# Kernel optimization log

Measured on AMD Instinct MI355X. Metric: run time of the kernel, lower is better.

## Reference

```python
import jax, jax.numpy as jnp
import numpy as np

# ---- constants (from init_kwargs / Config) ----
C = 10            # number of classes
P = 128           # fixed prototype capacity per class (masked)
GAMMA = 0.1
B_CONST = 10.0    # b
TAO = 1.0
BETA = 1.0
LAMBDA = 0.1
THRESHOLD = 40.0
EPS = 1e-6        # nn.PairwiseDistance eps (added to the difference)


def setup_inputs() -> dict:
    key = jax.random.key(0)
    k1, k2 = jax.random.split(key)
    features = jax.random.normal(k1, (8192, 512), dtype=jnp.float32)
    labels = jax.random.randint(k2, (8192,), 0, C, dtype=jnp.int32)
    return {"features": features, "labels": labels}


def _assign_prototypes(features, labels):
    """Sequential prototype assignment (faithful to assign_prototype).
    Fixed-capacity store: protos [C,P,D], counts [C,P], nproto [C]."""
    D = features.shape[1]
    protos = jnp.zeros((C, P, D), features.dtype)
    counts = jnp.zeros((C, P), jnp.int32)
    nproto = jnp.zeros((C,), jnp.int32)

    def step(carry, xs):
        protos, counts, nproto = carry
        f, l = xs
        row = protos[l]                       # [P, D]
        cnt = counts[l]                       # [P]
        n = nproto[l]
        valid = jnp.arange(P) < n
        d2 = jnp.sum((f[None, :] - row + EPS) ** 2, axis=-1)
        d2m = jnp.where(valid, d2, jnp.inf)
        idx = jnp.argmin(d2m)
        dmin = jnp.sqrt(d2m[idx])
        do_update = (n > 0) & (dmin < THRESHOLD)
        # running-mean update of closest prototype
        c = cnt[idx].astype(f.dtype)
        new_val = (row[idx] * c + f) / (c + 1.0)
        app_idx = jnp.minimum(n, P - 1)       # append slot (clamped; never hit with these settings)
        tgt_idx = jnp.where(do_update, idx, app_idx)
        tgt_val = jnp.where(do_update, new_val, f)
        tgt_cnt = jnp.where(do_update, cnt[idx] + 1, 1)
        row = row.at[tgt_idx].set(tgt_val)
        cnt = cnt.at[tgt_idx].set(tgt_cnt)
        n = jnp.where(do_update, n, jnp.minimum(n + 1, P))
        protos = protos.at[l].set(row)
        counts = counts.at[l].set(cnt)
        nproto = nproto.at[l].set(n)
        return (protos, counts, nproto), None

    (protos, counts, nproto), _ = jax.lax.scan(step, (protos, counts, nproto), (features, labels))
    return protos, nproto


def _forward(features, labels):
    # assign_prototype uses tensor(features).detach() -> stop_gradient
    protos, nproto = _assign_prototypes(jax.lax.stop_gradient(features), labels)
    B, D = features.shape
    flat = protos.reshape(C * P, D)
    valid = (jnp.arange(P)[None, :] < nproto[:, None]).reshape(C * P)

    # squared PairwiseDistance with eps added to the difference:
    # sum((f - p + eps)^2) = |f|^2 + |p|^2 - 2 f.p + 2*eps*(sum f - sum p) + D*eps^2
    f2 = jnp.sum(features ** 2, axis=-1)          # [B]
    p2 = jnp.sum(flat ** 2, axis=-1)              # [C*P]
    sf = jnp.sum(features, axis=-1)
    sp = jnp.sum(flat, axis=-1)
    d2 = (f2[:, None] + p2[None, :] - 2.0 * (features @ flat.T)
          + 2.0 * EPS * (sf[:, None] - sp[None, :]) + D * EPS * EPS)
    d2 = jnp.maximum(d2, 0.0)                     # [B, C*P]

    # dce loss: probability = 1e-6 + sum_label exp(-g d^2) / sum_all exp(-g d^2)
    expv = jnp.where(valid[None, :], jnp.exp(-GAMMA * d2), 0.0)
    per_class = expv.reshape(B, C, P).sum(-1)     # [B, C]
    one = per_class.sum(-1)                       # [B]
    num = jnp.take_along_axis(per_class, labels[:, None].astype(jnp.int32), axis=1)[:, 0]
    prob = 1e-6 + jnp.where(one > 0.0, num / one, one)
    dce_loss = jnp.sum(-jnp.log(prob))

    # pairwise loss: per sample, per existing class, min distance
    d2c = jnp.where(valid[None, :], d2, jnp.inf).reshape(B, C, P).min(-1)
    dmin = jnp.sqrt(d2c)                          # [B, C]
    sign = jnp.where(labels[:, None] == jnp.arange(C)[None, :], 1.0, -1.0)
    z = B_CONST - (TAO - dmin) * sign
    g = jnp.where(z > 10.0, z, jax.nn.softplus(BETA * z) / BETA)
    exists = nproto > 0                           # only classes present in all_prototypes
    pw_loss = jnp.sum(jnp.where(exists[None, :], g, 0.0))

    return dce_loss + LAMBDA * pw_loss


def reference(features, labels):
    return _forward(features, labels)
```

## Files before the change

### kernel.cpp

```cpp
#include <hip/hip_runtime.h>
#include <math.h>

#define NC 10
#define NP 128
#define ND 512
#define GAMMA  0.1f
#define BCONST 10.0f
#define TAO    1.0f
#define LAMBDA 0.1f
#define THR2   1600.0f
#define FEPS   1e-6f
#define NLDS   12
#define CH     16
#define MAXCH  512
#define IMAX   0x7FFFFFFF

__device__ __forceinline__ float allred64(float v) {
#pragma unroll
  for (int m = 1; m < 64; m <<= 1) v += __shfl_xor(v, m, 64);
  return v;
}

__global__ __launch_bounds__(256)
void ord_kernel(const int* __restrict__ labels, int B,
                int* __restrict__ order, int* __restrict__ cls_base,
                int* __restrict__ cls_cnt, int* __restrict__ fail_pos,
                int* __restrict__ nproto_g, float* __restrict__ out)
{
  __shared__ int lab[8192];
  __shared__ int wtot[4][NC];
  const int t = threadIdx.x, lane = t & 63, w = t >> 6;

  if (t < NC) { fail_pos[t] = IMAX; nproto_g[t] = 0; }
  if (t == 0) out[0] = 0.f;

  const int4* lp = (const int4*)labels;
  for (int i = t; i < (B >> 2); i += 256) {
    int4 v = lp[i];
    lab[i*4+0] = v.x; lab[i*4+1] = v.y; lab[i*4+2] = v.z; lab[i*4+3] = v.w;
  }
  for (int i = (B & ~3) + t; i < B; i += 256) lab[i] = labels[i];
  __syncthreads();

  const int segsz = (B + 255) >> 8;
  const int s0 = t * segsz, s1 = min(s0 + segsz, B);

  int loc[NC];
#pragma unroll
  for (int c = 0; c < NC; ++c) loc[c] = 0;
  for (int i = s0; i < s1; ++i) {
    int l = lab[i];
#pragma unroll
    for (int c = 0; c < NC; ++c) loc[c] += (l == c) ? 1 : 0;
  }

  int pre[NC];
#pragma unroll
  for (int c = 0; c < NC; ++c) pre[c] = loc[c];
#pragma unroll
  for (int m = 1; m < 64; m <<= 1) {
#pragma unroll
    for (int c = 0; c < NC; ++c) {
      int u = __shfl_up(pre[c], m, 64);
      if (lane >= m) pre[c] += u;
    }
  }
  if (lane == 63) {
#pragma unroll
    for (int c = 0; c < NC; ++c) wtot[w][c] = pre[c];
  }
  __syncthreads();

  int pos[NC];
  {
    int cb = 0;
#pragma unroll
    for (int c = 0; c < NC; ++c) {
      int tot = wtot[0][c] + wtot[1][c] + wtot[2][c] + wtot[3][c];
      int before = 0;
#pragma unroll
      for (int ww = 0; ww < 4; ++ww) before += (ww < w) ? wtot[ww][c] : 0;
      pos[c] = cb + before + (pre[c] - loc[c]);
      if (t == 0) { cls_base[c] = cb; cls_cnt[c] = tot; }
      cb += tot;
    }
  }

  for (int i = s0; i < s1; ++i) {
    int l = lab[i];
#pragma unroll
    for (int c = 0; c < NC; ++c)
      if (l == c) order[pos[c]++] = i;
  }
}

__global__ __launch_bounds__(64)
void chunksum_kernel(const float* __restrict__ feats, const int* __restrict__ order,
                     const int* __restrict__ cls_base, const int* __restrict__ cls_cnt,
                     float* __restrict__ chunksum)
{
  const int c = blockIdx.x / MAXCH, g = blockIdx.x % MAXCH;
  const int cnt = cls_cnt[c];
  const int nch = (cnt + CH - 1) / CH;
  if (g >= nch) return;
  const int base = cls_base[c], lane = threadIdx.x;
  const int k0 = g * CH, k1 = min(k0 + CH, cnt);
  int myidx = (lane < CH && k0 + lane < cnt) ? order[base + k0 + lane] : 0;

  float S[8] = {0, 0, 0, 0, 0, 0, 0, 0};
  int k = k0;
  for (; k + 4 <= k1; k += 4) {
    float4 A[4], Bv[4];
#pragma unroll
    for (int j = 0; j < 4; ++j) {
      int idx = __shfl(myidx, k + j - k0, 64);
      const float4* fp = (const float4*)(feats + (size_t)idx * ND + lane * 8);
      A[j] = fp[0]; Bv[j] = fp[1];
    }
#pragma unroll
    for (int j = 0; j < 4; ++j) {
      S[0]+=A[j].x; S[1]+=A[j].y; S[2]+=A[j].z; S[3]+=A[j].w;
      S[4]+=Bv[j].x; S[5]+=Bv[j].y; S[6]+=Bv[j].z; S[7]+=Bv[j].w;
    }
  }
  for (; k < k1; ++k) {
    int idx = __shfl(myidx, k - k0, 64);
    const float4* fp = (const float4*)(feats + (size_t)idx * ND + lane * 8);
    float4 a = fp[0], b = fp[1];
    S[0]+=a.x; S[1]+=a.y; S[2]+=a.z; S[3]+=a.w;
    S[4]+=b.x; S[5]+=b.y; S[6]+=b.z; S[7]+=b.w;
  }
  float4* cp = (float4*)(chunksum + ((size_t)c * MAXCH + g) * ND + lane * 8);
  cp[0] = make_float4(S[0], S[1], S[2], S[3]);
  cp[1] = make_float4(S[4], S[5], S[6], S[7]);
}

__global__ __launch_bounds__(64)
void verify_kernel(const float* __restrict__ feats, const int* __restrict__ order,
                   const int* __restrict__ cls_base, const int* __restrict__ cls_cnt,
                   const float* __restrict__ chunksum, int* __restrict__ fail_pos,
                   float* __restrict__ gproto, float* __restrict__ p2s,
                   float* __restrict__ sps, int* __restrict__ nproto_g)
{
  const int c = blockIdx.x / MAXCH, g = blockIdx.x % MAXCH;
  const int cnt = cls_cnt[c];
  const int nch = (cnt + CH - 1) / CH;
  if (g >= nch) return;
  const int base = cls_base[c], lane = threadIdx.x;
  const int k0 = g * CH, k1 = min(k0 + CH, cnt);
  int myidx = (lane < CH && k0 + lane < cnt) ? order[base + k0 + lane] : 0;

  float P[8] = {0, 0, 0, 0, 0, 0, 0, 0};
  {
    const float* cbase = chunksum + (size_t)c * MAXCH * ND + lane * 8;
    int j = 0;
    for (; j + 4 <= g; j += 4) {
      float4 A[4], Bv[4];
#pragma unroll
      for (int q = 0; q < 4; ++q) {
        const float4* pp = (const float4*)(cbase + (size_t)(j + q) * ND);
        A[q] = pp[0]; Bv[q] = pp[1];
      }
#pragma unroll
      for (int q = 0; q < 4; ++q) {
        P[0]+=A[q].x; P[1]+=A[q].y; P[2]+=A[q].z; P[3]+=A[q].w;
        P[4]+=Bv[q].x; P[5]+=Bv[q].y; P[6]+=Bv[q].z; P[7]+=Bv[q].w;
      }
    }
    for (; j < g; ++j) {
      const float4* pp = (const float4*)(cbase + (size_t)j * ND);
      float4 a = pp[0], b = pp[1];
      P[0]+=a.x; P[1]+=a.y; P[2]+=a.z; P[3]+=a.w;
      P[4]+=b.x; P[5]+=b.y; P[6]+=b.z; P[7]+=b.w;
    }
  }

  int k = k0;
  for (; k + 4 <= k1; k += 4) {
    float4 A[4], Bv[4];
#pragma unroll
    for (int j = 0; j < 4; ++j) {
      int idx = __shfl(myidx, k + j - k0, 64);
      const float4* fp = (const float4*)(feats + (size_t)idx * ND + lane * 8);
      A[j] = fp[0]; Bv[j] = fp[1];
    }
    float part[4];
#pragma unroll
    for (int j = 0; j < 4; ++j) {
      int kk = k + j;
      float f[8] = {A[j].x, A[j].y, A[j].z, A[j].w, Bv[j].x, Bv[j].y, Bv[j].z, Bv[j].w};
      if (kk > 0) {
        float inv = 1.f / (float)kk;
        float p = 0.f;
#pragma unroll
        for (int e = 0; e < 8; ++e) { float d = f[e] - P[e] * inv + FEPS; p += d * d; }
        part[j] = p;
      } else part[j] = 0.f;
#pragma unroll
      for (int e = 0; e < 8; ++e) P[e] += f[e];
    }
#pragma unroll
    for (int m = 1; m < 64; m <<= 1) {
#pragma unroll
      for (int j = 0; j < 4; ++j) part[j] += __shfl_xor(part[j], m, 64);
    }
    if (lane == 0) {
#pragma unroll
      for (int j = 0; j < 4; ++j) {
        int kk = k + j;
        if (kk > 0 && !(part[j] < THR2)) atomicMin(&fail_pos[c], kk);
      }
    }
  }
  for (; k < k1; ++k) {
    int idx = __shfl(myidx, k - k0, 64);
    const float4* fp = (const float4*)(feats + (size_t)idx * ND + lane * 8);
    float4 fa = fp[0], fb = fp[1];
    float f[8] = {fa.x, fa.y, fa.z, fa.w, fb.x, fb.y, fb.z, fb.w};
    if (k > 0) {
      float inv = 1.f / (float)k;
      float p = 0.f;
#pragma unroll
      for (int e = 0; e < 8; ++e) { float d = f[e] - P[e] * inv + FEPS; p += d * d; }
      float d2 = allred64(p);
      if (!(d2 < THR2) && lane == 0) atomicMin(&fail_pos[c], k);
    }
#pragma unroll
    for (int e = 0; e < 8; ++e) P[e] += f[e];
  }

  if (g == nch - 1) {
    float inv = 1.f / (float)cnt;
    float p[8];
#pragma unroll
    for (int e = 0; e < 8; ++e) p[e] = P[e] * inv;
    float4* gp = (float4*)(gproto + (size_t)c * NP * ND + lane * 8);
    gp[0] = make_float4(p[0], p[1], p[2], p[3]);
    gp[1] = make_float4(p[4], p[5], p[6], p[7]);
    float P2p = 0.f, SPp = 0.f;
#pragma unroll
    for (int e = 0; e < 8; ++e) { P2p += p[e]*p[e]; SPp += p[e]; }
    float P2 = allred64(P2p), SP = allred64(SPp);
    if (lane == 0) { p2s[c*NP] = P2; sps[c*NP] = SP; nproto_g[c] = 1; }
  }
}

__global__ __launch_bounds__(64)
void fallback_kernel(const float* __restrict__ feats, const int* __restrict__ order,
                     const int* __restrict__ cls_base, const int* __restrict__ cls_cnt,
                     const int* __restrict__ fail_pos,
                     float* __restrict__ gproto, float* __restrict__ p2s,
                     float* __restrict__ sps, int* __restrict__ nproto_g)
{
  const int c = blockIdx.x;
  if (fail_pos[c] == IMAX) return;

  __shared__ float ls_proto[NLDS][ND];
  __shared__ int   ls_cnt[NP];
  const int lane = threadIdx.x;
  const int base = cls_base[c], cnt = cls_cnt[c];

  float p0[8];
  int cnt0 = 0, n = 0;
  float fA[8], fB[8], fC[8];

  auto LOADF = [&](float (&buf)[8], int m) {
    int idx = order[base + m];
    const float4* fp = (const float4*)(feats + (size_t)idx * ND + lane * 8);
    float4 a = fp[0], b = fp[1];
    buf[0]=a.x; buf[1]=a.y; buf[2]=a.z; buf[3]=a.w;
    buf[4]=b.x; buf[5]=b.y; buf[6]=b.z; buf[7]=b.w;
  };

  auto STEP = [&](float (&f)[8]) {
    float best = 3.4e38f;
    int bidx = 0;
    if (n > 0) {
      float part = 0.f;
#pragma unroll
      for (int e = 0; e < 8; ++e) { float d = f[e] - p0[e] + FEPS; part += d * d; }
      best = allred64(part);
      for (int j = 1; j < n; ++j) {
        float pj[8];
        if (j <= NLDS) {
          const float4* pp = (const float4*)(&ls_proto[j-1][lane*8]);
          float4 a = pp[0], b = pp[1];
          pj[0]=a.x; pj[1]=a.y; pj[2]=a.z; pj[3]=a.w;
          pj[4]=b.x; pj[5]=b.y; pj[6]=b.z; pj[7]=b.w;
        } else {
          const float4* pp = (const float4*)(gproto + ((size_t)c*NP + j)*ND + lane*8);
          float4 a = pp[0], b = pp[1];
          pj[0]=a.x; pj[1]=a.y; pj[2]=a.z; pj[3]=a.w;
          pj[4]=b.x; pj[5]=b.y; pj[6]=b.z; pj[7]=b.w;
        }
        float part2 = 0.f;
#pragma unroll
        for (int e = 0; e < 8; ++e) { float d = f[e] - pj[e] + FEPS; part2 += d * d; }
        float tot = allred64(part2);
        if (tot < best) { best = tot; bidx = j; }
      }
    }
    if (n > 0 && best < THR2) {
      if (bidx == 0) {
        float cc = (float)cnt0, inv = 1.f / (cc + 1.f);
#pragma unroll
        for (int e = 0; e < 8; ++e) p0[e] = (p0[e]*cc + f[e]) * inv;
        cnt0++;
      } else {
        int ci = ls_cnt[bidx];
        float cc = (float)ci, inv = 1.f / (cc + 1.f);
        if (bidx <= NLDS) {
          float* row = &ls_proto[bidx-1][lane*8];
#pragma unroll
          for (int e = 0; e < 8; ++e) row[e] = (row[e]*cc + f[e]) * inv;
        } else {
          float* row = gproto + ((size_t)c*NP + bidx)*ND + lane*8;
#pragma unroll
          for (int e = 0; e < 8; ++e) row[e] = (row[e]*cc + f[e]) * inv;
        }
        if (lane == 0) ls_cnt[bidx] = ci + 1;
      }
    } else {
      int app = min(n, NP - 1);
      if (app == 0) {
#pragma unroll
        for (int e = 0; e < 8; ++e) p0[e] = f[e];
        cnt0 = 1;
      } else if (app <= NLDS) {
        float* row = &ls_proto[app-1][lane*8];
#pragma unroll
        for (int e = 0; e < 8; ++e) row[e] = f[e];
        if (lane == 0) ls_cnt[app] = 1;
      } else {
        float* row = gproto + ((size_t)c*NP + app)*ND + lane*8;
#pragma unroll
        for (int e = 0; e < 8; ++e) row[e] = f[e];
        if (lane == 0) ls_cnt[app] = 1;
      }
      n = min(n + 1, NP);
    }
  };

  if (cnt > 0) LOADF(fA, 0);
  if (cnt > 1) LOADF(fB, 1);
  if (cnt > 2) LOADF(fC, 2);
  int m = 0;
  while (m < cnt) {
    STEP(fA); ++m; if (m + 2 < cnt) LOADF(fA, m + 2);
    if (m >= cnt) break;
    STEP(fB); ++m; if (m + 2 < cnt) LOADF(fB, m + 2);
    if (m >= cnt) break;
    STEP(fC); ++m; if (m + 2 < cnt) LOADF(fC, m + 2);
  }

  for (int j = 0; j < n; ++j) {
    float pj[8];
    if (j == 0) {
#pragma unroll
      for (int e = 0; e < 8; ++e) pj[e] = p0[e];
    } else if (j <= NLDS) {
      const float4* pp = (const float4*)(&ls_proto[j-1][lane*8]);
      float4 a = pp[0], b = pp[1];
      pj[0]=a.x; pj[1]=a.y; pj[2]=a.z; pj[3]=a.w;
      pj[4]=b.x; pj[5]=b.y; pj[6]=b.z; pj[7]=b.w;
    } else {
      const float4* pp = (const float4*)(gproto + ((size_t)c*NP + j)*ND + lane*8);
      float4 a = pp[0], b = pp[1];
      pj[0]=a.x; pj[1]=a.y; pj[2]=a.z; pj[3]=a.w;
      pj[4]=b.x; pj[5]=b.y; pj[6]=b.z; pj[7]=b.w;
    }
    float4* gp = (float4*)(gproto + ((size_t)c*NP + j)*ND + lane*8);
    gp[0] = make_float4(pj[0], pj[1], pj[2], pj[3]);
    gp[1] = make_float4(pj[4], pj[5], pj[6], pj[7]);
    float P2p = 0.f, SPp = 0.f;
#pragma unroll
    for (int e = 0; e < 8; ++e) { P2p += pj[e]*pj[e]; SPp += pj[e]; }
    float P2 = allred64(P2p), SP = allred64(SPp);
    if (lane == 0) { p2s[c*NP + j] = P2; sps[c*NP + j] = SP; }
  }
  if (lane == 0) nproto_g[c] = n;
}

__global__ __launch_bounds__(256)
void loss_kernel(const float* __restrict__ feats, const int* __restrict__ labels, int B,
                 const float* __restrict__ gproto, const float* __restrict__ p2s,
                 const float* __restrict__ sps, const int* __restrict__ nproto_g,
                 float* __restrict__ out)
{
  __shared__ float bsum[4];
  const int lane = threadIdx.x & 63;
  const int wid  = threadIdx.x >> 6;
  const int gw   = blockIdx.x * 4 + wid;
  const int nw   = gridDim.x * 4;

  int np[NC];
  bool fast = true;
#pragma unroll
  for (int cc = 0; cc < NC; ++cc) { np[cc] = nproto_g[cc]; fast &= (np[cc] == 1); }

  float acc = 0.f;

  if (fast) {
    float p2v[NC], spv[NC];
#pragma unroll
    for (int cc = 0; cc < NC; ++cc) { p2v[cc] = p2s[cc*NP]; spv[cc] = sps[cc*NP]; }

    for (int b = gw; b < B; b += nw) {
      const float4* fp = (const float4*)(feats + (size_t)b * ND + lane * 8);
      float4 a4 = fp[0], b4 = fp[1];
      float f[8] = {a4.x, a4.y, a4.z, a4.w, b4.x, b4.y, b4.z, b4.w};
      int lab = labels[b];

      float v[12];
#pragma unroll
      for (int cc = 0; cc < NC; ++cc) {
        const float4* pp = (const float4*)(gproto + (size_t)cc * NP * ND + lane * 8);
        float4 pa = pp[0], pb = pp[1];
        v[cc] = f[0]*pa.x + f[1]*pa.y + f[2]*pa.z + f[3]*pa.w
              + f[4]*pb.x + f[5]*pb.y + f[6]*pb.z + f[7]*pb.w;
      }
      float f2p = 0.f, sfp = 0.f;
#pragma unroll
      for (int e = 0; e < 8; ++e) { f2p += f[e]*f[e]; sfp += f[e]; }
      v[10] = f2p; v[11] = sfp;

#pragma unroll
      for (int m = 1; m < 64; m <<= 1) {
#pragma unroll
        for (int q = 0; q < 12; ++q) v[q] += __shfl_xor(v[q], m, 64);
      }
      float f2 = v[10], sf = v[11];

      float one = 0.f, num = 0.f, pw = 0.f;
#pragma unroll
      for (int cc = 0; cc < NC; ++cc) {
        float d2 = f2 + p2v[cc] - 2.f*v[cc]
                 + 2.f*FEPS*(sf - spv[cc]) + (float)ND*FEPS*FEPS;
        d2 = fmaxf(d2, 0.f);
        float e = expf(-GAMMA * d2);
        one += e;
        if (cc == lab) num = e;
        float dmin = sqrtf(d2);
        float sign = (cc == lab) ? 1.f : -1.f;
        float z = BCONST - (TAO - dmin) * sign;
        float gg = (z > 10.f) ? z : log1pf(expf(z));
        pw += gg;
      }
      float prob = 1e-6f + ((one > 0.f) ? num / one : one);
      acc += -logf(prob) + LAMBDA * pw;
    }
  } else {
    for (int b = gw; b < B; b += nw) {
      const float4* fp = (const float4*)(feats + (size_t)b * ND + lane * 8);
      float4 a4 = fp[0], b4 = fp[1];
      float f[8] = {a4.x, a4.y, a4.z, a4.w, b4.x, b4.y, b4.z, b4.w};
      float f2p = 0.f, sfp = 0.f;
#pragma unroll
      for (int e = 0; e < 8; ++e) { f2p += f[e]*f[e]; sfp += f[e]; }
      float f2 = allred64(f2p);
      float sf = allred64(sfp);
      int lab = labels[b];

      float one = 0.f, num = 0.f, pw = 0.f;
      for (int cc = 0; cc < NC; ++cc) {
        int nn = np[cc];
        if (nn <= 0) continue;
        float sume = 0.f, bestd2 = 3.4e38f;
        for (int j = 0; j < nn; ++j) {
          const float4* pp = (const float4*)(gproto + ((size_t)cc*NP + j)*ND + lane*8);
          float4 pa = pp[0], pb = pp[1];
          float dp = f[0]*pa.x + f[1]*pa.y + f[2]*pa.z + f[3]*pa.w
                   + f[4]*pb.x + f[5]*pb.y + f[6]*pb.z + f[7]*pb.w;
          float dot = allred64(dp);
          float d2 = f2 + p2s[cc*NP + j] - 2.f*dot
                   + 2.f*FEPS*(sf - sps[cc*NP + j]) + (float)ND*FEPS*FEPS;
          d2 = fmaxf(d2, 0.f);
          sume  += expf(-GAMMA * d2);
          bestd2 = fminf(bestd2, d2);
        }
        one += sume;
        if (cc == lab) num = sume;
        float dmin = sqrtf(bestd2);
        float sign = (cc == lab) ? 1.f : -1.f;
        float z = BCONST - (TAO - dmin) * sign;
        float g = (z > 10.f) ? z : log1pf(expf(z));
        pw += g;
      }
      float prob = 1e-6f + ((one > 0.f) ? num / one : one);
      acc += -logf(prob) + LAMBDA * pw;
    }
  }

  if (lane == 0) bsum[wid] = acc;
  __syncthreads();
  if (threadIdx.x == 0) atomicAdd(out, bsum[0] + bsum[1] + bsum[2] + bsum[3]);
}

extern "C" void kernel_launch(void* const* d_in, const int* in_sizes, int n_in,
                              void* d_out, int out_size, void* d_ws, size_t ws_size,
                              hipStream_t stream) {
  const float* feats  = (const float*)d_in[0];
  const int*   labels = (const int*)d_in[1];
  int B = in_sizes[0] / ND;

  float* gproto   = (float*)d_ws;
  float* p2s      = gproto + (size_t)NC * NP * ND;
  float* sps      = p2s + NC * NP;
  float* chunksum = sps + NC * NP;
  int*   nproto_g = (int*)(chunksum + (size_t)NC * MAXCH * ND);
  int*   order    = nproto_g + NC;
  int*   cls_base = order + B;
  int*   cls_cnt  = cls_base + NC;
  int*   fail_pos = cls_cnt + NC;

  hipLaunchKernelGGL(ord_kernel, dim3(1), dim3(256), 0, stream,
                     labels, B, order, cls_base, cls_cnt, fail_pos,
                     nproto_g, (float*)d_out);
  hipLaunchKernelGGL(chunksum_kernel, dim3(NC * MAXCH), dim3(64), 0, stream,
                     feats, order, cls_base, cls_cnt, chunksum);
  hipLaunchKernelGGL(verify_kernel, dim3(NC * MAXCH), dim3(64), 0, stream,
                     feats, order, cls_base, cls_cnt, chunksum, fail_pos,
                     gproto, p2s, sps, nproto_g);
  hipLaunchKernelGGL(fallback_kernel, dim3(NC), dim3(64), 0, stream,
                     feats, order, cls_base, cls_cnt, fail_pos,
                     gproto, p2s, sps, nproto_g);
  hipLaunchKernelGGL(loss_kernel, dim3(2048), dim3(256), 0, stream,
                     feats, labels, B, gproto, p2s, sps, nproto_g, (float*)d_out);
}
```

Before: 88.82 us.

## Fuse five-kernel pipeline into one cooperative persistent kernel with grid syncs

Replaces the five separate launches (ordering, chunk sums, verify, fallback, loss) with a single cooperative kernel of 256 blocks that separates the phases with grid.sync. Chunk work is compacted into a flat list indexed by per-class chunk bases, so no waves are spent on empty chunk slots. This removes launch gaps and idle blocks between phases. The cost is grid-wide barriers, only 1024 waves for the loss phase, and a serial ordering phase on block 0 while the other blocks wait. The old multi-kernel path stays as a fallback if the cooperative launch fails.

```diff
diff --git a/kernel.cpp b/kernel.cpp
--- a/kernel.cpp
+++ b/kernel.cpp
@@ -1,5 +1,8 @@
 #include <hip/hip_runtime.h>
+#include <hip/hip_cooperative_groups.h>
 #include <math.h>
+
+namespace cg = cooperative_groups;
 
 #define NC 10
 #define NP 128
@@ -14,11 +17,474 @@
 #define CH     16
 #define MAXCH  512
 #define IMAX   0x7FFFFFFF
-
-__device__ __forceinline__ float allred64(float v) {
+#define NBLK   256
+#define NWAVES (NBLK * 4)
+
+__device__ __forceinline__ float allredf(float v) {
 #pragma unroll
   for (int m = 1; m < 64; m <<= 1) v += __shfl_xor(v, m, 64);
   return v;
+}
+
+struct SOrd { int lab[8192]; int wtot[4][NC]; };
+struct SFb  { float ls_proto[NLDS][ND]; int ls_cnt[NP]; };
+union  SMem { SOrd ord; SFb fb; };
+
+__global__ __launch_bounds__(256, 2)
+void fused_kernel(const float* __restrict__ feats, const int* __restrict__ labels, int B,
+                  float* __restrict__ gproto, float* __restrict__ p2s, float* __restrict__ sps,
+                  float* __restrict__ chunksum,
+                  int* __restrict__ cls_base, int* __restrict__ cls_cnt,
+                  int* __restrict__ chunk_base, int* __restrict__ nchtot_g,
+                  int* __restrict__ fail_pos, int* __restrict__ nproto_g,
+                  int* __restrict__ order, float* __restrict__ out)
+{
+  cg::grid_group grid = cg::this_grid();
+  __shared__ SMem sm;
+  __shared__ float bsum[4];
+
+  const int t = threadIdx.x, lane = t & 63, wid = t >> 6;
+  const int gwid = blockIdx.x * 4 + wid;
+
+  if (blockIdx.x == 0) {
+    const int w = wid;
+    if (t < NC) { fail_pos[t] = IMAX; nproto_g[t] = 0; }
+    if (t == 0) out[0] = 0.f;
+
+    const int4* lp = (const int4*)labels;
+    for (int i = t; i < (B >> 2); i += 256) {
+      int4 v = lp[i];
+      sm.ord.lab[i*4+0] = v.x; sm.ord.lab[i*4+1] = v.y;
+      sm.ord.lab[i*4+2] = v.z; sm.ord.lab[i*4+3] = v.w;
+    }
+    for (int i = (B & ~3) + t; i < B; i += 256) sm.ord.lab[i] = labels[i];
+    __syncthreads();
+
+    const int segsz = (B + 255) >> 8;
+    const int s0 = t * segsz, s1 = min(s0 + segsz, B);
+
+    int loc[NC];
+#pragma unroll
+    for (int c = 0; c < NC; ++c) loc[c] = 0;
+    for (int i = s0; i < s1; ++i) {
+      int l = sm.ord.lab[i];
+#pragma unroll
+      for (int c = 0; c < NC; ++c) loc[c] += (l == c) ? 1 : 0;
+    }
+
+    int pre[NC];
+#pragma unroll
+    for (int c = 0; c < NC; ++c) pre[c] = loc[c];
+#pragma unroll
+    for (int m = 1; m < 64; m <<= 1) {
+#pragma unroll
+      for (int c = 0; c < NC; ++c) {
+        int u = __shfl_up(pre[c], m, 64);
+        if (lane >= m) pre[c] += u;
+      }
+    }
+    if (lane == 63) {
+#pragma unroll
+      for (int c = 0; c < NC; ++c) sm.ord.wtot[w][c] = pre[c];
+    }
+    __syncthreads();
+
+    int pos[NC];
+    {
+      int cb = 0, crun = 0;
+#pragma unroll
+      for (int c = 0; c < NC; ++c) {
+        int tot = sm.ord.wtot[0][c] + sm.ord.wtot[1][c] + sm.ord.wtot[2][c] + sm.ord.wtot[3][c];
+        int before = 0;
+#pragma unroll
+        for (int ww = 0; ww < 4; ++ww) before += (ww < w) ? sm.ord.wtot[ww][c] : 0;
+        pos[c] = cb + before + (pre[c] - loc[c]);
+        if (t == 0) { cls_base[c] = cb; cls_cnt[c] = tot; chunk_base[c] = crun; }
+        cb += tot;
+        crun += (tot + CH - 1) / CH;
+      }
+      if (t == 0) nchtot_g[0] = crun;
+    }
+
+    for (int i = s0; i < s1; ++i) {
+      int l = sm.ord.lab[i];
+#pragma unroll
+      for (int c = 0; c < NC; ++c)
+        if (l == c) order[pos[c]++] = i;
+    }
+  }
+  grid.sync();
+
+  int chbv[NC];
+#pragma unroll
+  for (int c = 0; c < NC; ++c) chbv[c] = chunk_base[c];
+  const int nchtot = nchtot_g[0];
+
+  for (int fid = gwid; fid < nchtot; fid += NWAVES) {
+    int c = 0;
+    while (c + 1 < NC && chbv[c + 1] <= fid) ++c;
+    const int g = fid - chbv[c];
+    const int cnt = cls_cnt[c], base = cls_base[c];
+    const int k0 = g * CH, k1 = min(k0 + CH, cnt);
+    int myidx = (lane < CH && k0 + lane < cnt) ? order[base + k0 + lane] : 0;
+
+    float S[8] = {0, 0, 0, 0, 0, 0, 0, 0};
+    int k = k0;
+    for (; k + 4 <= k1; k += 4) {
+      float4 A[4], Bv[4];
+#pragma unroll
+      for (int j = 0; j < 4; ++j) {
+        int idx = __shfl(myidx, k + j - k0, 64);
+        const float4* fp = (const float4*)(feats + (size_t)idx * ND + lane * 8);
+        A[j] = fp[0]; Bv[j] = fp[1];
+      }
+#pragma unroll
+      for (int j = 0; j < 4; ++j) {
+        S[0]+=A[j].x; S[1]+=A[j].y; S[2]+=A[j].z; S[3]+=A[j].w;
+        S[4]+=Bv[j].x; S[5]+=Bv[j].y; S[6]+=Bv[j].z; S[7]+=Bv[j].w;
+      }
+    }
+    for (; k < k1; ++k) {
+      int idx = __shfl(myidx, k - k0, 64);
+      const float4* fp = (const float4*)(feats + (size_t)idx * ND + lane * 8);
+      float4 a = fp[0], b = fp[1];
+      S[0]+=a.x; S[1]+=a.y; S[2]+=a.z; S[3]+=a.w;
+      S[4]+=b.x; S[5]+=b.y; S[6]+=b.z; S[7]+=b.w;
+    }
+    float4* cp = (float4*)(chunksum + (size_t)fid * ND + lane * 8);
+    cp[0] = make_float4(S[0], S[1], S[2], S[3]);
+    cp[1] = make_float4(S[4], S[5], S[6], S[7]);
+  }
+  grid.sync();
+
+  for (int fid = gwid; fid < nchtot; fid += NWAVES) {
+    int c = 0;
+    while (c + 1 < NC && chbv[c + 1] <= fid) ++c;
+    const int g = fid - chbv[c];
+    const int cnt = cls_cnt[c], base = cls_base[c];
+    const int nch = (cnt + CH - 1) / CH;
+    const int k0 = g * CH, k1 = min(k0 + CH, cnt);
+    int myidx = (lane < CH && k0 + lane < cnt) ? order[base + k0 + lane] : 0;
+
+    float P[8] = {0, 0, 0, 0, 0, 0, 0, 0};
+    {
+      const float* cbase = chunksum + (size_t)chbv[c] * ND + lane * 8;
+      int j = 0;
+      for (; j + 4 <= g; j += 4) {
+        float4 A[4], Bv[4];
+#pragma unroll
+        for (int q = 0; q < 4; ++q) {
+          const float4* pp = (const float4*)(cbase + (size_t)(j + q) * ND);
+          A[q] = pp[0]; Bv[q] = pp[1];
+        }
+#pragma unroll
+        for (int q = 0; q < 4; ++q) {
+          P[0]+=A[q].x; P[1]+=A[q].y; P[2]+=A[q].z; P[3]+=A[q].w;
+          P[4]+=Bv[q].x; P[5]+=Bv[q].y; P[6]+=Bv[q].z; P[7]+=Bv[q].w;
+        }
+      }
+      for (; j < g; ++j) {
+        const float4* pp = (const float4*)(cbase + (size_t)j * ND);
+        float4 a = pp[0], b = pp[1];
+        P[0]+=a.x; P[1]+=a.y; P[2]+=a.z; P[3]+=a.w;
+        P[4]+=b.x; P[5]+=b.y; P[6]+=b.z; P[7]+=b.w;
+      }
+    }
+
+    int k = k0;
+    for (; k + 4 <= k1; k += 4) {
+      float4 A[4], Bv[4];
+#pragma unroll
+      for (int j = 0; j < 4; ++j) {
+        int idx = __shfl(myidx, k + j - k0, 64);
+        const float4* fp = (const float4*)(feats + (size_t)idx * ND + lane * 8);
+        A[j] = fp[0]; Bv[j] = fp[1];
+      }
+      float part[4];
+#pragma unroll
+      for (int j = 0; j < 4; ++j) {
+        int kk = k + j;
+        float f[8] = {A[j].x, A[j].y, A[j].z, A[j].w, Bv[j].x, Bv[j].y, Bv[j].z, Bv[j].w};
+        if (kk > 0) {
+          float inv = 1.f / (float)kk;
+          float p = 0.f;
+#pragma unroll
+          for (int e = 0; e < 8; ++e) { float d = f[e] - P[e] * inv + FEPS; p += d * d; }
+          part[j] = p;
+        } else part[j] = 0.f;
+#pragma unroll
+        for (int e = 0; e < 8; ++e) P[e] += f[e];
+      }
+#pragma unroll
+      for (int m = 1; m < 64; m <<= 1) {
+#pragma unroll
+        for (int j = 0; j < 4; ++j) part[j] += __shfl_xor(part[j], m, 64);
+      }
+      if (lane == 0) {
+#pragma unroll
+        for (int j = 0; j < 4; ++j) {
+          int kk = k + j;
+          if (kk > 0 && !(part[j] < THR2)) atomicMin(&fail_pos[c], kk);
+        }
+      }
+    }
+    for (; k < k1; ++k) {
+      int idx = __shfl(myidx, k - k0, 64);
+      const float4* fp = (const float4*)(feats + (size_t)idx * ND + lane * 8);
+      float4 fa = fp[0], fb = fp[1];
+      float f[8] = {fa.x, fa.y, fa.z, fa.w, fb.x, fb.y, fb.z, fb.w};
+      if (k > 0) {
+        float inv = 1.f / (float)k;
+        float p = 0.f;
+#pragma unroll
+        for (int e = 0; e < 8; ++e) { float d = f[e] - P[e] * inv + FEPS; p += d * d; }
+        float d2 = allredf(p);
+        if (!(d2 < THR2) && lane == 0) atomicMin(&fail_pos[c], k);
+      }
+#pragma unroll
+      for (int e = 0; e < 8; ++e) P[e] += f[e];
+    }
+
+    if (g == nch - 1 && cnt > 0) {
+      float inv = 1.f / (float)cnt;
+      float p[8];
+#pragma unroll
+      for (int e = 0; e < 8; ++e) p[e] = P[e] * inv;
+      float4* gp = (float4*)(gproto + (size_t)c * NP * ND + lane * 8);
+      gp[0] = make_float4(p[0], p[1], p[2], p[3]);
+      gp[1] = make_float4(p[4], p[5], p[6], p[7]);
+      float P2p = 0.f, SPp = 0.f;
+#pragma unroll
+      for (int e = 0; e < 8; ++e) { P2p += p[e]*p[e]; SPp += p[e]; }
+      float P2 = allredf(P2p), SP = allredf(SPp);
+      if (lane == 0) { p2s[c*NP] = P2; sps[c*NP] = SP; nproto_g[c] = 1; }
+    }
+  }
+  grid.sync();
+
+  if (wid == 0 && blockIdx.x < NC && fail_pos[blockIdx.x] != IMAX) {
+    const int c = blockIdx.x;
+    const int base = cls_base[c], cnt = cls_cnt[c];
+    float p0[8];
+    int cnt0 = 0, n = 0;
+    float fA[8], fB[8], fC[8];
+
+    auto LOADF = [&](float (&buf)[8], int m) {
+      int idx = order[base + m];
+      const float4* fp = (const float4*)(feats + (size_t)idx * ND + lane * 8);
+      float4 a = fp[0], b = fp[1];
+      buf[0]=a.x; buf[1]=a.y; buf[2]=a.z; buf[3]=a.w;
+      buf[4]=b.x; buf[5]=b.y; buf[6]=b.z; buf[7]=b.w;
+    };
+    auto STEP = [&](float (&f)[8]) {
+      float best = 3.4e38f;
+      int bidx = 0;
+      if (n > 0) {
+        float part = 0.f;
+#pragma unroll
+        for (int e = 0; e < 8; ++e) { float d = f[e] - p0[e] + FEPS; part += d * d; }
+        best = allredf(part);
+        for (int j = 1; j < n; ++j) {
+          float pj[8];
+          if (j <= NLDS) {
+            const float4* pp = (const float4*)(&sm.fb.ls_proto[j-1][lane*8]);
+            float4 a = pp[0], b = pp[1];
+            pj[0]=a.x; pj[1]=a.y; pj[2]=a.z; pj[3]=a.w;
+            pj[4]=b.x; pj[5]=b.y; pj[6]=b.z; pj[7]=b.w;
+          } else {
+            const float4* pp = (const float4*)(gproto + ((size_t)c*NP + j)*ND + lane*8);
+            float4 a = pp[0], b = pp[1];
+            pj[0]=a.x; pj[1]=a.y; pj[2]=a.z; pj[3]=a.w;
+            pj[4]=b.x; pj[5]=b.y; pj[6]=b.z; pj[7]=b.w;
+          }
+          float part2 = 0.f;
+#pragma unroll
+          for (int e = 0; e < 8; ++e) { float d = f[e] - pj[e] + FEPS; part2 += d * d; }
+          float tot = allredf(part2);
+          if (tot < best) { best = tot; bidx = j; }
+        }
+      }
+      if (n > 0 && best < THR2) {
+        if (bidx == 0) {
+          float cc = (float)cnt0, inv = 1.f / (cc + 1.f);
+#pragma unroll
+          for (int e = 0; e < 8; ++e) p0[e] = (p0[e]*cc + f[e]) * inv;
+          cnt0++;
+        } else {
+          int ci = sm.fb.ls_cnt[bidx];
+          float cc = (float)ci, inv = 1.f / (cc + 1.f);
+          if (bidx <= NLDS) {
+            float* row = &sm.fb.ls_proto[bidx-1][lane*8];
+#pragma unroll
+            for (int e = 0; e < 8; ++e) row[e] = (row[e]*cc + f[e]) * inv;
+          } else {
+            float* row = gproto + ((size_t)c*NP + bidx)*ND + lane*8;
+#pragma unroll
+            for (int e = 0; e < 8; ++e) row[e] = (row[e]*cc + f[e]) * inv;
+          }
+          if (lane == 0) sm.fb.ls_cnt[bidx] = ci + 1;
+        }
+      } else {
+        int app = min(n, NP - 1);
+        if (app == 0) {
+#pragma unroll
+          for (int e = 0; e < 8; ++e) p0[e] = f[e];
+          cnt0 = 1;
+        } else if (app <= NLDS) {
+          float* row = &sm.fb.ls_proto[app-1][lane*8];
+#pragma unroll
+          for (int e = 0; e < 8; ++e) row[e] = f[e];
+          if (lane == 0) sm.fb.ls_cnt[app] = 1;
+        } else {
+          float* row = gproto + ((size_t)c*NP + app)*ND + lane*8;
+#pragma unroll
+          for (int e = 0; e < 8; ++e) row[e] = f[e];
+          if (lane == 0) sm.fb.ls_cnt[app] = 1;
+        }
+        n = min(n + 1, NP);
+      }
+    };
+
+    if (cnt > 0) LOADF(fA, 0);
+    if (cnt > 1) LOADF(fB, 1);
+    if (cnt > 2) LOADF(fC, 2);
+    int m = 0;
+    while (m < cnt) {
+      STEP(fA); ++m; if (m + 2 < cnt) LOADF(fA, m + 2);
+      if (m >= cnt) break;
+      STEP(fB); ++m; if (m + 2 < cnt) LOADF(fB, m + 2);
+      if (m >= cnt) break;
+      STEP(fC); ++m; if (m + 2 < cnt) LOADF(fC, m + 2);
+    }
+
+    for (int j = 0; j < n; ++j) {
+      float pj[8];
+      if (j == 0) {
+#pragma unroll
+        for (int e = 0; e < 8; ++e) pj[e] = p0[e];
+      } else if (j <= NLDS) {
+        const float4* pp = (const float4*)(&sm.fb.ls_proto[j-1][lane*8]);
+        float4 a = pp[0], b = pp[1];
+        pj[0]=a.x; pj[1]=a.y; pj[2]=a.z; pj[3]=a.w;
+        pj[4]=b.x; pj[5]=b.y; pj[6]=b.z; pj[7]=b.w;
+      } else {
+        const float4* pp = (const float4*)(gproto + ((size_t)c*NP + j)*ND + lane*8);
+        float4 a = pp[0], b = pp[1];
+        pj[0]=a.x; pj[1]=a.y; pj[2]=a.z; pj[3]=a.w;
+        pj[4]=b.x; pj[5]=b.y; pj[6]=b.z; pj[7]=b.w;
+      }
+      float4* gp = (float4*)(gproto + ((size_t)c*NP + j)*ND + lane*8);
+      gp[0] = make_float4(pj[0], pj[1], pj[2], pj[3]);
+      gp[1] = make_float4(pj[4], pj[5], pj[6], pj[7]);
+      float P2p = 0.f, SPp = 0.f;
+#pragma unroll
+      for (int e = 0; e < 8; ++e) { P2p += pj[e]*pj[e]; SPp += pj[e]; }
+      float P2 = allredf(P2p), SP = allredf(SPp);
+      if (lane == 0) { p2s[c*NP + j] = P2; sps[c*NP + j] = SP; }
+    }
+    if (lane == 0) nproto_g[c] = n;
+  }
+  grid.sync();
+
+  {
+    int np[NC]; bool fast = true;
+#pragma unroll
+    for (int cc = 0; cc < NC; ++cc) { np[cc] = nproto_g[cc]; fast &= (np[cc] == 1); }
+    float acc = 0.f;
+
+    if (fast) {
+      float p2v[NC], spv[NC];
+#pragma unroll
+      for (int cc = 0; cc < NC; ++cc) { p2v[cc] = p2s[cc*NP]; spv[cc] = sps[cc*NP]; }
+      for (int b = gwid; b < B; b += NWAVES) {
+        const float4* fp = (const float4*)(feats + (size_t)b * ND + lane * 8);
+        float4 a4 = fp[0], b4 = fp[1];
+        float f[8] = {a4.x, a4.y, a4.z, a4.w, b4.x, b4.y, b4.z, b4.w};
+        int lab = labels[b];
+
+        float v[12];
+#pragma unroll
+        for (int cc = 0; cc < NC; ++cc) {
+          const float4* pp = (const float4*)(gproto + (size_t)cc * NP * ND + lane * 8);
+          float4 pa = pp[0], pb = pp[1];
+          v[cc] = f[0]*pa.x + f[1]*pa.y + f[2]*pa.z + f[3]*pa.w
+                + f[4]*pb.x + f[5]*pb.y + f[6]*pb.z + f[7]*pb.w;
+        }
+        float f2p = 0.f, sfp = 0.f;
+#pragma unroll
+        for (int e = 0; e < 8; ++e) { f2p += f[e]*f[e]; sfp += f[e]; }
+        v[10] = f2p; v[11] = sfp;
+#pragma unroll
+        for (int m = 1; m < 64; m <<= 1) {
+#pragma unroll
+          for (int q = 0; q < 12; ++q) v[q] += __shfl_xor(v[q], m, 64);
+        }
+        float f2 = v[10], sf = v[11];
+
+        float one = 0.f, num = 0.f, pw = 0.f;
+#pragma unroll
+        for (int cc = 0; cc < NC; ++cc) {
+          float d2 = f2 + p2v[cc] - 2.f*v[cc]
+                   + 2.f*FEPS*(sf - spv[cc]) + (float)ND*FEPS*FEPS;
+          d2 = fmaxf(d2, 0.f);
+          float e = expf(-GAMMA * d2);
+          one += e;
+          if (cc == lab) num = e;
+          float dmin = sqrtf(d2);
+          float sign = (cc == lab) ? 1.f : -1.f;
+          float z = BCONST - (TAO - dmin) * sign;
+          float gg = (z > 10.f) ? z : log1pf(expf(z));
+          pw += gg;
+        }
+        float prob = 1e-6f + ((one > 0.f) ? num / one : one);
+        acc += -logf(prob) + LAMBDA * pw;
+      }
+    } else {
+      for (int b = gwid; b < B; b += NWAVES) {
+        const float4* fp = (const float4*)(feats + (size_t)b * ND + lane * 8);
+        float4 a4 = fp[0], b4 = fp[1];
+        float f[8] = {a4.x, a4.y, a4.z, a4.w, b4.x, b4.y, b4.z, b4.w};
+        float f2p = 0.f, sfp = 0.f;
+#pragma unroll
+        for (int e = 0; e < 8; ++e) { f2p += f[e]*f[e]; sfp += f[e]; }
+        float f2 = allredf(f2p);
+        float sf = allredf(sfp);
+        int lab = labels[b];
+
+        float one = 0.f, num = 0.f, pw = 0.f;
+        for (int cc = 0; cc < NC; ++cc) {
+          int nn = np[cc];
+          if (nn <= 0) continue;
+          float sume = 0.f, bestd2 = 3.4e38f;
+          for (int j = 0; j < nn; ++j) {
+            const float4* pp = (const float4*)(gproto + ((size_t)cc*NP + j)*ND + lane*8);
+            float4 pa = pp[0], pb = pp[1];
+            float dp = f[0]*pa.x + f[1]*pa.y + f[2]*pa.z + f[3]*pa.w
+                     + f[4]*pb.x + f[5]*pb.y + f[6]*pb.z + f[7]*pb.w;
+            float dot = allredf(dp);
+            float d2 = f2 + p2s[cc*NP + j] - 2.f*dot
+                     + 2.f*FEPS*(sf - sps[cc*NP + j]) + (float)ND*FEPS*FEPS;
+            d2 = fmaxf(d2, 0.f);
+            sume  += expf(-GAMMA * d2);
+            bestd2 = fminf(bestd2, d2);
+          }
+          one += sume;
+          if (cc == lab) num = sume;
+          float dmin = sqrtf(bestd2);
+          float sign = (cc == lab) ? 1.f : -1.f;
+          float z = BCONST - (TAO - dmin) * sign;
+          float g = (z > 10.f) ? z : log1pf(expf(z));
+          pw += g;
+        }
+        float prob = 1e-6f + ((one > 0.f) ? num / one : one);
+        acc += -logf(prob) + LAMBDA * pw;
+      }
+    }
+
+    if (lane == 0) bsum[wid] = acc;
+    __syncthreads();
+    if (t == 0) atomicAdd(out, bsum[0] + bsum[1] + bsum[2] + bsum[3]);
+  }
 }
 
 __global__ __launch_bounds__(256)
@@ -85,7 +551,6 @@
       cb += tot;
     }
   }
-
   for (int i = s0; i < s1; ++i) {
     int l = lab[i];
 #pragma unroll
@@ -222,7 +687,7 @@
       float p = 0.f;
 #pragma unroll
       for (int e = 0; e < 8; ++e) { float d = f[e] - P[e] * inv + FEPS; p += d * d; }
-      float d2 = allred64(p);
+      float d2 = allredf(p);
       if (!(d2 < THR2) && lane == 0) atomicMin(&fail_pos[c], k);
     }
 #pragma unroll
@@ -240,7 +705,7 @@
     float P2p = 0.f, SPp = 0.f;
 #pragma unroll
     for (int e = 0; e < 8; ++e) { P2p += p[e]*p[e]; SPp += p[e]; }
-    float P2 = allred64(P2p), SP = allred64(SPp);
+    float P2 = allredf(P2p), SP = allredf(SPp);
     if (lane == 0) { p2s[c*NP] = P2; sps[c*NP] = SP; nproto_g[c] = 1; }
   }
 }
@@ -271,7 +736,6 @@
     buf[0]=a.x; buf[1]=a.y; buf[2]=a.z; buf[3]=a.w;
     buf[4]=b.x; buf[5]=b.y; buf[6]=b.z; buf[7]=b.w;
   };
-
   auto STEP = [&](float (&f)[8]) {
     float best = 3.4e38f;
     int bidx = 0;
@@ -279,7 +743,7 @@
       float part = 0.f;
 #pragma unroll
       for (int e = 0; e < 8; ++e) { float d = f[e] - p0[e] + FEPS; part += d * d; }
-      best = allred64(part);
+      best = allredf(part);
       for (int j = 1; j < n; ++j) {
         float pj[8];
         if (j <= NLDS) {
@@ -296,7 +760,7 @@
         float part2 = 0.f;
 #pragma unroll
         for (int e = 0; e < 8; ++e) { float d = f[e] - pj[e] + FEPS; part2 += d * d; }
-        float tot = allred64(part2);
+        float tot = allredf(part2);
         if (tot < best) { best = tot; bidx = j; }
       }
     }
@@ -375,7 +839,7 @@
     float P2p = 0.f, SPp = 0.f;
 #pragma unroll
     for (int e = 0; e < 8; ++e) { P2p += pj[e]*pj[e]; SPp += pj[e]; }
-    float P2 = allred64(P2p), SP = allred64(SPp);
+    float P2 = allredf(P2p), SP = allredf(SPp);
     if (lane == 0) { p2s[c*NP + j] = P2; sps[c*NP + j] = SP; }
   }
   if (lane == 0) nproto_g[c] = n;
@@ -399,18 +863,15 @@
   for (int cc = 0; cc < NC; ++cc) { np[cc] = nproto_g[cc]; fast &= (np[cc] == 1); }
 
   float acc = 0.f;
-
   if (fast) {
     float p2v[NC], spv[NC];
 #pragma unroll
     for (int cc = 0; cc < NC; ++cc) { p2v[cc] = p2s[cc*NP]; spv[cc] = sps[cc*NP]; }
-
     for (int b = gw; b < B; b += nw) {
       const float4* fp = (const float4*)(feats + (size_t)b * ND + lane * 8);
       float4 a4 = fp[0], b4 = fp[1];
       float f[8] = {a4.x, a4.y, a4.z, a4.w, b4.x, b4.y, b4.z, b4.w};
       int lab = labels[b];
-
       float v[12];
 #pragma unroll
       for (int cc = 0; cc < NC; ++cc) {
@@ -423,14 +884,12 @@
 #pragma unroll
       for (int e = 0; e < 8; ++e) { f2p += f[e]*f[e]; sfp += f[e]; }
       v[10] = f2p; v[11] = sfp;
-
 #pragma unroll
       for (int m = 1; m < 64; m <<= 1) {
 #pragma unroll
         for (int q = 0; q < 12; ++q) v[q] += __shfl_xor(v[q], m, 64);
       }
       float f2 = v[10], sf = v[11];
-
       float one = 0.f, num = 0.f, pw = 0.f;
 #pragma unroll
       for (int cc = 0; cc < NC; ++cc) {
@@ -457,10 +916,9 @@
       float f2p = 0.f, sfp = 0.f;
 #pragma unroll
       for (int e = 0; e < 8; ++e) { f2p += f[e]*f[e]; sfp += f[e]; }
-      float f2 = allred64(f2p);
-      float sf = allred64(sfp);
+      float f2 = allredf(f2p);
+      float sf = allredf(sfp);
       int lab = labels[b];
-
       float one = 0.f, num = 0.f, pw = 0.f;
       for (int cc = 0; cc < NC; ++cc) {
         int nn = np[cc];
@@ -471,7 +929,7 @@
           float4 pa = pp[0], pb = pp[1];
           float dp = f[0]*pa.x + f[1]*pa.y + f[2]*pa.z + f[3]*pa.w
                    + f[4]*pb.x + f[5]*pb.y + f[6]*pb.z + f[7]*pb.w;
-          float dot = allred64(dp);
+          float dot = allredf(dp);
           float d2 = f2 + p2s[cc*NP + j] - 2.f*dot
                    + 2.f*FEPS*(sf - sps[cc*NP + j]) + (float)ND*FEPS*FEPS;
           d2 = fmaxf(d2, 0.f);
@@ -512,18 +970,31 @@
   int*   cls_base = order + B;
   int*   cls_cnt  = cls_base + NC;
   int*   fail_pos = cls_cnt + NC;
-
-  hipLaunchKernelGGL(ord_kernel, dim3(1), dim3(256), 0, stream,
-                     labels, B, order, cls_base, cls_cnt, fail_pos,
-                     nproto_g, (float*)d_out);
-  hipLaunchKernelGGL(chunksum_kernel, dim3(NC * MAXCH), dim3(64), 0, stream,
-                     feats, order, cls_base, cls_cnt, chunksum);
-  hipLaunchKernelGGL(verify_kernel, dim3(NC * MAXCH), dim3(64), 0, stream,
-                     feats, order, cls_base, cls_cnt, chunksum, fail_pos,
-                     gproto, p2s, sps, nproto_g);
-  hipLaunchKernelGGL(fallback_kernel, dim3(NC), dim3(64), 0, stream,
-                     feats, order, cls_base, cls_cnt, fail_pos,
-                     gproto, p2s, sps, nproto_g);
-  hipLaunchKernelGGL(loss_kernel, dim3(2048), dim3(256), 0, stream,
-                     feats, labels, B, gproto, p2s, sps, nproto_g, (float*)d_out);
+  int*   chunk_base = fail_pos + NC;
+  int*   nchtot_g = chunk_base + NC;
+  float* outf     = (float*)d_out;
+
+  void* args[] = { (void*)&feats, (void*)&labels, (void*)&B,
+                   (void*)&gproto, (void*)&p2s, (void*)&sps, (void*)&chunksum,
+                   (void*)&cls_base, (void*)&cls_cnt, (void*)&chunk_base,
+                   (void*)&nchtot_g, (void*)&fail_pos, (void*)&nproto_g,
+                   (void*)&order, (void*)&outf };
+  hipError_t err = hipLaunchCooperativeKernel((const void*)fused_kernel,
+                                              dim3(NBLK), dim3(256), args, 0, stream);
+  if (err != hipSuccess) {
+    (void)hipGetLastError();
+    hipLaunchKernelGGL(ord_kernel, dim3(1), dim3(256), 0, stream,
+                       labels, B, order, cls_base, cls_cnt, fail_pos,
+                       nproto_g, outf);
+    hipLaunchKernelGGL(chunksum_kernel, dim3(NC * MAXCH), dim3(64), 0, stream,
+                       feats, order, cls_base, cls_cnt, chunksum);
+    hipLaunchKernelGGL(verify_kernel, dim3(NC * MAXCH), dim3(64), 0, stream,
+                       feats, order, cls_base, cls_cnt, chunksum, fail_pos,
+                       gproto, p2s, sps, nproto_g);
+    hipLaunchKernelGGL(fallback_kernel, dim3(NC), dim3(64), 0, stream,
+                       feats, order, cls_base, cls_cnt, fail_pos,
+                       gproto, p2s, sps, nproto_g);
+    hipLaunchKernelGGL(loss_kernel, dim3(2048), dim3(256), 0, stream,
+                       feats, labels, B, gproto, p2s, sps, nproto_g, outf);
+  }
 }
```

Result: slower. 189.8 us (+113.7%).
